# Kernel optimization log

Hardware: AMD Instinct MI355X
Metric: run time of the kernel (lower is better)

Reference implementation:

```python
import math
import jax, jax.numpy as jnp
import numpy as np

H = 16  # number of heads

def setup_inputs() -> dict:
    key0 = jax.random.key(0)
    ks = jax.random.split(key0, 8)
    B, S, D = 4, 2048, 1024
    query = jax.random.normal(ks[0], (B, S, D), dtype=jnp.float32)
    key_t = jax.random.normal(ks[1], (B, S, D), dtype=jnp.float32)
    value = jax.random.normal(ks[2], (B, S, D), dtype=jnp.float32)
    mask = jax.random.randint(ks[3], (B, S, S), 0, 2, dtype=jnp.int32)
    scale = 1.0 / math.sqrt(D)
    Wq = jax.random.normal(ks[4], (D, D), dtype=jnp.float32) * scale
    Wk = jax.random.normal(ks[5], (D, D), dtype=jnp.float32) * scale
    Wv = jax.random.normal(ks[6], (D, D), dtype=jnp.float32) * scale
    Wo = jax.random.normal(ks[7], (D, D), dtype=jnp.float32) * scale
    return {"query": query, "key": key_t, "value": value, "mask": mask,
            "Wq": Wq, "Wk": Wk, "Wv": Wv, "Wo": Wo}


def reference(query, key, value, mask, Wq, Wk, Wv, Wo):
    B, S, D = query.shape
    dk = D // H
    # Linear projections (nn.Linear, no bias): x @ W.T, then split heads
    def proj(x, W):
        return (x @ W.T).reshape(B, -1, H, dk).transpose(0, 2, 1, 3)  # [B,H,S,dk]
    q = proj(query, Wq)
    k = proj(key, Wk)
    v = proj(value, Wv)
    scores = jnp.einsum('bhqd,bhkd->bhqk', q, k) / math.sqrt(dk)
    m = mask[:, None, :, :] != 0  # [B,1,Sq,Sk] broadcast over heads
    scores = jnp.where(m, scores, jnp.float32(-1e9))
    p = jax.nn.softmax(scores, axis=-1)
    p = jnp.where(m, p, 0.0)
    # dropout is identity in eval mode
    x = jnp.einsum('bhqk,bhkd->bhqd', p, v)
    x = x.transpose(0, 2, 1, 3).reshape(B, -1, D)
    return x @ Wo.T
```

## Files before the change

kernel.cpp:

```cpp
#include <hip/hip_runtime.h>
#include <hip/hip_bf16.h>
#include <stdint.h>
#include <stddef.h>

typedef __bf16 bf16_t;
typedef __bf16 bf16x8 __attribute__((ext_vector_type(8)));
typedef __bf16 bf16x4 __attribute__((ext_vector_type(4)));
typedef float floatx4 __attribute__((ext_vector_type(4)));
typedef float floatx16 __attribute__((ext_vector_type(16)));

#define D_MODEL 1024
#define SEQ 2048
#define NB 4
#define NH 16
#define DK 64
#define MTOT 8192

#define QSCALE 0.1803368801111204f
#define FMAX 14.0f

__device__ inline bf16x8 ld8f(const float* p) {
  float4 a = *(const float4*)p;
  float4 b = *(const float4*)(p + 4);
  bf16x8 v;
  v[0] = (bf16_t)a.x; v[1] = (bf16_t)a.y; v[2] = (bf16_t)a.z; v[3] = (bf16_t)a.w;
  v[4] = (bf16_t)b.x; v[5] = (bf16_t)b.y; v[6] = (bf16_t)b.z; v[7] = (bf16_t)b.w;
  return v;
}

typedef const __attribute__((address_space(1))) unsigned int gu32;
typedef __attribute__((address_space(3))) unsigned int lu32;
__device__ static inline void async_copy16(const void* g, void* l) {
  __builtin_amdgcn_global_load_lds((gu32*)g, (lu32*)l, 16, 0, 0);
}

__device__ static inline uint32_t cvtpk_bf16(float lo, float hi) {
  uint32_t r;
  asm("v_cvt_pk_bf16_f32 %0, %1, %2" : "=v"(r) : "v"(lo), "v"(hi));
  return r;
}

__global__ __launch_bounds__(256) void prep_kernel(
    const float* __restrict__ q, const float* __restrict__ k,
    const float* __restrict__ v, const float* __restrict__ Wq,
    const float* __restrict__ Wk, const float* __restrict__ Wv,
    const int* __restrict__ mask, bf16_t* __restrict__ qb,
    bf16_t* __restrict__ kb, bf16_t* __restrict__ vb,
    bf16_t* __restrict__ wqb, bf16_t* __restrict__ wkb,
    bf16_t* __restrict__ wvb, uint32_t* __restrict__ bits) {
  size_t c = (size_t)blockIdx.x * 256 + threadIdx.x;
  const float* src;
  bf16_t* dst;
  size_t off;
  if (c < 1048576) { src = q; dst = qb; off = c; }
  else if (c < 2097152) { src = k; dst = kb; off = c - 1048576; }
  else if (c < 3145728) { src = v; dst = vb; off = c - 2097152; }
  else if (c < 3276800) { src = Wq; dst = wqb; off = c - 3145728; }
  else if (c < 3407872) { src = Wk; dst = wkb; off = c - 3276800; }
  else { src = Wv; dst = wvb; off = c - 3407872; }
  size_t e = off * 8;
  *(bf16x8*)&dst[e] = ld8f(&src[e]);

  const int lane = threadIdx.x & 63;
  const size_t w0 = c >> 6;
  const size_t nw = ((size_t)gridDim.x * 256) >> 6;
  const size_t total = (size_t)NB * SEQ * SEQ / 64;
  for (size_t i = w0; i < total; i += nw) {
    int mv = mask[i * 64 + lane];
    unsigned long long b = __ballot(mv != 0);
    if (lane == 0) *(unsigned long long*)&bits[i * 2] = b;
  }
}

__global__ __launch_bounds__(256) void cvt_w_kernel(const float* __restrict__ W,
                                                    bf16_t* __restrict__ wb) {
  size_t e = ((size_t)blockIdx.x * 256 + threadIdx.x) * 8;
  *(bf16x8*)&wb[e] = ld8f(&W[e]);
}

#define BM 64
#define BN 128
#define BK 64

template <int MODE, typename TC>
__global__ __launch_bounds__(256) void gemm_bt(const bf16_t* __restrict__ A,
                                               const bf16_t* __restrict__ W,
                                               TC* __restrict__ C, float scale) {
  __shared__ __align__(16) bf16_t As[BM * BK];
  __shared__ __align__(16) bf16_t Bs[BN * BK];
  const int tid = threadIdx.x;
  const int lane = tid & 63;
  const int wave = tid >> 6;
  const int row0 = blockIdx.x * BM;
  const int col0 = blockIdx.y * BN;
  const int wr = (wave >> 1) * 32;
  const int wc = (wave & 1) * 64;
  const int lrow = lane & 15;
  const int quad = lane >> 4;
  const int srow = lane >> 3;
  const int scol = ((lane & 7) ^ srow) * 8;

  floatx4 acc[2][4] = {};

  for (int k0 = 0; k0 < D_MODEL; k0 += BK) {
#pragma unroll
    for (int it = 0; it < 2; it++) {
      int seg = wave * 2 + it;
      async_copy16(&A[(size_t)(row0 + seg * 8 + srow) * D_MODEL + k0 + scol],
                   &As[seg * 512]);
    }
#pragma unroll
    for (int it = 0; it < 4; it++) {
      int seg = wave * 4 + it;
      async_copy16(&W[(size_t)(col0 + seg * 8 + srow) * D_MODEL + k0 + scol],
                   &Bs[seg * 512]);
    }
    __syncthreads();
#pragma unroll
    for (int kk = 0; kk < BK; kk += 32) {
      bf16x8 af[2], bfr[4];
#pragma unroll
      for (int i = 0; i < 2; i++)
        af[i] = *(const bf16x8*)&As[(wr + i * 16 + lrow) * BK +
                                    (((kk >> 3) + quad) ^ (lane & 7)) * 8];
#pragma unroll
      for (int j = 0; j < 4; j++)
        bfr[j] = *(const bf16x8*)&Bs[(wc + j * 16 + lrow) * BK +
                                     (((kk >> 3) + quad) ^ (lane & 7)) * 8];
#pragma unroll
      for (int i = 0; i < 2; i++)
#pragma unroll
        for (int j = 0; j < 4; j++)
          acc[i][j] = __builtin_amdgcn_mfma_f32_16x16x32_bf16(af[i], bfr[j],
                                                              acc[i][j], 0, 0, 0);
    }
    __syncthreads();
  }

#pragma unroll
  for (int i = 0; i < 2; i++) {
#pragma unroll
    for (int j = 0; j < 4; j++) {
      int gr0 = row0 + wr + i * 16 + quad * 4;
      int gc = col0 + wc + j * 16 + lrow;
      if (MODE == 1) {
        int b = gr0 >> 11;
        int s = gr0 & (SEQ - 1);
        bf16x4 v;
#pragma unroll
        for (int r = 0; r < 4; r++) v[r] = (bf16_t)(acc[i][j][r] * scale);
        *(bf16x4*)&C[((size_t)(b * D_MODEL + gc)) * SEQ + s] = v;
      } else {
#pragma unroll
        for (int r = 0; r < 4; r++)
          C[(size_t)(gr0 + r) * D_MODEL + gc] = (TC)(acc[i][j][r] * scale);
      }
    }
  }
}

__global__ __launch_bounds__(256) void attn_kernel(
    const bf16_t* __restrict__ Q, const bf16_t* __restrict__ K,
    const bf16_t* __restrict__ Vt, const uint32_t* __restrict__ bits,
    bf16_t* __restrict__ X) {
  __shared__ __align__(16) bf16_t Ks[128 * DK];
  __shared__ __align__(16) bf16_t Vs[DK * 128];
  const int tid = threadIdx.x;
  const int lane = tid & 63;
  const int wave = tid >> 6;
  const int l31 = lane & 31;
  const int half = lane >> 5;
  const int lrow16 = lane & 15;
  const int bh = blockIdx.x & 63;
  const int qbase = (blockIdx.x >> 6) * 128;
  const int b = bh >> 4;
  const int h = bh & 15;
  const int q0w = qbase + wave * 32;
  const int srow8 = lane >> 3;
  const int scol8 = ((lane & 7) ^ srow8) * 8;
  const int vrow = lane >> 4;

  bf16x8 qf[4];
#pragma unroll
  for (int kst = 0; kst < 4; kst++)
    qf[kst] = *(const bf16x8*)&Q[((size_t)(b * SEQ + q0w + l31)) * D_MODEL +
                                 h * DK + kst * 16 + half * 8];

  bf16x8 ones;
#pragma unroll
  for (int e = 0; e < 8; e++) ones[e] = (bf16_t)1.0f;

  const int kfbase = (l31 * 64) ^ ((lane & 7) * 8) ^ (half * 8);
  const int vfbase = (l31 * 128) ^ (lrow16 * 8) ^ (half * 8);

  floatx16 O0 = {}, O1 = {}, lsum = {};

  for (int kt = 0; kt < SEQ / 128; kt++) {
    const int kbase = kt * 128;
    const uint4 m4 =
        *(const uint4*)&bits[((size_t)(b * SEQ + q0w + l31)) * 64 + kt * 4];
    const uint32_t mwa[4] = {m4.x, m4.y, m4.z, m4.w};
    __syncthreads();
#pragma unroll
    for (int it = 0; it < 4; it++) {
      int seg = wave * 4 + it;
      async_copy16(&K[((size_t)(b * SEQ + kbase + seg * 8 + srow8)) * D_MODEL +
                      h * DK + scol8],
                   &Ks[seg * 512]);
    }
#pragma unroll
    for (int it = 0; it < 4; it++) {
      int seg = wave * 4 + it;
      int d = seg * 4 + vrow;
      async_copy16(&Vt[((size_t)(b * D_MODEL + h * DK + d)) * SEQ + kbase +
                       ((lrow16 ^ (d & 15)) * 8)],
                   &Vs[seg * 512]);
    }
    __syncthreads();

#pragma unroll
    for (int t = 0; t < 4; t++) {
      floatx16 s;
#pragma unroll
      for (int r = 0; r < 16; r++) s[r] = -FMAX;
#pragma unroll
      for (int kst = 0; kst < 4; kst++) {
        bf16x8 kf =
            *(const bf16x8*)&Ks[t * 2048 + (kfbase ^ (kst * 16))];
        s = __builtin_amdgcn_mfma_f32_32x32x16_bf16(kf, qf[kst], s, 0, 0, 0);
      }
      const uint32_t wh = mwa[t] >> (half * 4);
#pragma unroll
      for (int r = 0; r < 16; r++) {
        float p = __builtin_amdgcn_exp2f(s[r]);
        s[r] = ((wh >> ((r & 3) + 8 * (r >> 2))) & 1u) ? p : 0.f;
      }
#pragma unroll
      for (int ks = 0; ks < 2; ks++) {
        uint32_t w0 = cvtpk_bf16(s[8 * ks + 0], s[8 * ks + 1]);
        uint32_t w2 = cvtpk_bf16(s[8 * ks + 4], s[8 * ks + 5]);
        uint32_t w1 = cvtpk_bf16(s[8 * ks + 2], s[8 * ks + 3]);
        uint32_t w3 = cvtpk_bf16(s[8 * ks + 6], s[8 * ks + 7]);
        asm("v_permlane32_swap_b32 %0, %1" : "+v"(w0), "+v"(w2));
        asm("v_permlane32_swap_b32 %0, %1" : "+v"(w1), "+v"(w3));
        union { uint32_t u[4]; bf16x8 v; } pa;
        pa.u[0] = w0; pa.u[1] = w1; pa.u[2] = w2; pa.u[3] = w3;
        bf16x8 vf0 =
            *(const bf16x8*)&Vs[vfbase ^ (t * 32 + ks * 16)];
        bf16x8 vf1 =
            *(const bf16x8*)&Vs[4096 + (vfbase ^ (t * 32 + ks * 16))];
        O0 = __builtin_amdgcn_mfma_f32_32x32x16_bf16(pa.v, vf0, O0, 0, 0, 0);
        O1 = __builtin_amdgcn_mfma_f32_32x32x16_bf16(pa.v, vf1, O1, 0, 0, 0);
        lsum = __builtin_amdgcn_mfma_f32_32x32x16_bf16(pa.v, ones, lsum, 0, 0, 0);
      }
    }
  }

#pragma unroll
  for (int r = 0; r < 16; r++) {
    int qrow = q0w + (r & 3) + 8 * (r >> 2) + 4 * half;
    float li = lsum[r];
    float inv = (li > 0.f) ? 1.f / li : 0.f;
    X[((size_t)(b * SEQ + qrow)) * D_MODEL + h * DK + l31] =
        (bf16_t)(O0[r] * inv);
    X[((size_t)(b * SEQ + qrow)) * D_MODEL + h * DK + 32 + l31] =
        (bf16_t)(O1[r] * inv);
  }
}

extern "C" void kernel_launch(void* const* d_in, const int* in_sizes, int n_in,
                              void* d_out, int out_size, void* d_ws,
                              size_t ws_size, hipStream_t stream) {
  const float* query = (const float*)d_in[0];
  const float* key = (const float*)d_in[1];
  const float* value = (const float*)d_in[2];
  const int* mask = (const int*)d_in[3];
  const float* Wq = (const float*)d_in[4];
  const float* Wk = (const float*)d_in[5];
  const float* Wv = (const float*)d_in[6];
  const float* Wo = (const float*)d_in[7];
  float* out = (float*)d_out;

  char* ws = (char*)d_ws;
  char* dob = (char*)d_out;
  bf16_t* qb = (bf16_t*)(ws);
  bf16_t* kb = (bf16_t*)(ws + ((size_t)16 << 20));
  bf16_t* vb = (bf16_t*)(ws + ((size_t)32 << 20));
  bf16_t* Kp = qb;
  bf16_t* Vtp = kb;
  bf16_t* Xp = vb;
  bf16_t* wob = (bf16_t*)ws;
  bf16_t* Qp = (bf16_t*)d_out;
  uint32_t* bits = (uint32_t*)(dob + ((size_t)16 << 20));
  bf16_t* wqb = (bf16_t*)(dob + ((size_t)18 << 20));
  bf16_t* wkb = (bf16_t*)(dob + ((size_t)20 << 20));
  bf16_t* wvb = (bf16_t*)(dob + ((size_t)22 << 20));

  prep_kernel<<<13824, 256, 0, stream>>>(query, key, value, Wq, Wk, Wv, mask,
                                         qb, kb, vb, wqb, wkb, wvb, bits);

  dim3 gg(MTOT / BM, D_MODEL / BN);
  gemm_bt<0, bf16_t><<<gg, 256, 0, stream>>>(qb, wqb, Qp, QSCALE);
  gemm_bt<0, bf16_t><<<gg, 256, 0, stream>>>(kb, wkb, Kp, 1.0f);
  gemm_bt<1, bf16_t><<<gg, 256, 0, stream>>>(vb, wvb, Vtp, 1.0f);
  attn_kernel<<<dim3(SEQ / 128 * NB * NH), 256, 0, stream>>>(Qp, Kp, Vtp, bits,
                                                             Xp);
  cvt_w_kernel<<<512, 256, 0, stream>>>(Wo, wob);
  gemm_bt<0, float><<<gg, 256, 0, stream>>>(Xp, wob, out, 1.0f);
}
```

Before: 400.4 us.

## Double-buffer LDS tiles in projection GEMM to overlap loads with MFMA

Splits the GEMM's LDS A/B tiles into two buffers and issues the async copies for the next K tile before computing on the current one. Uses an explicit vmcnt wait (6 outstanding copies) plus barriers, which replaces the two full syncthreads per iteration. The goal is to hide global-to-LDS latency behind MFMA work, at the cost of twice the LDS per block, which may lower occupancy. The manual vmcnt count depends on the exact number of copies per thread.

```diff
diff --git a/kernel.cpp b/kernel.cpp
--- a/kernel.cpp
+++ b/kernel.cpp
@@ -86,8 +86,8 @@
 __global__ __launch_bounds__(256) void gemm_bt(const bf16_t* __restrict__ A,
                                                const bf16_t* __restrict__ W,
                                                TC* __restrict__ C, float scale) {
-  __shared__ __align__(16) bf16_t As[BM * BK];
-  __shared__ __align__(16) bf16_t Bs[BN * BK];
+  __shared__ __align__(16) bf16_t As[2][BM * BK];
+  __shared__ __align__(16) bf16_t Bs[2][BN * BK];
   const int tid = threadIdx.x;
   const int lane = tid & 63;
   const int wave = tid >> 6;
@@ -102,31 +102,33 @@
 
   floatx4 acc[2][4] = {};
 
-  for (int k0 = 0; k0 < D_MODEL; k0 += BK) {
+  auto stage = [&](int buf, int k0) {
 #pragma unroll
     for (int it = 0; it < 2; it++) {
       int seg = wave * 2 + it;
       async_copy16(&A[(size_t)(row0 + seg * 8 + srow) * D_MODEL + k0 + scol],
-                   &As[seg * 512]);
+                   &As[buf][seg * 512]);
     }
 #pragma unroll
     for (int it = 0; it < 4; it++) {
       int seg = wave * 4 + it;
       async_copy16(&W[(size_t)(col0 + seg * 8 + srow) * D_MODEL + k0 + scol],
-                   &Bs[seg * 512]);
-    }
-    __syncthreads();
+                   &Bs[buf][seg * 512]);
+    }
+  };
+
+  auto compute = [&](int buf) {
 #pragma unroll
     for (int kk = 0; kk < BK; kk += 32) {
       bf16x8 af[2], bfr[4];
 #pragma unroll
       for (int i = 0; i < 2; i++)
-        af[i] = *(const bf16x8*)&As[(wr + i * 16 + lrow) * BK +
-                                    (((kk >> 3) + quad) ^ (lane & 7)) * 8];
+        af[i] = *(const bf16x8*)&As[buf][(wr + i * 16 + lrow) * BK +
+                                        (((kk >> 3) + quad) ^ (lane & 7)) * 8];
 #pragma unroll
       for (int j = 0; j < 4; j++)
-        bfr[j] = *(const bf16x8*)&Bs[(wc + j * 16 + lrow) * BK +
-                                     (((kk >> 3) + quad) ^ (lane & 7)) * 8];
+        bfr[j] = *(const bf16x8*)&Bs[buf][(wc + j * 16 + lrow) * BK +
+                                         (((kk >> 3) + quad) ^ (lane & 7)) * 8];
 #pragma unroll
       for (int i = 0; i < 2; i++)
 #pragma unroll
@@ -134,8 +136,24 @@
           acc[i][j] = __builtin_amdgcn_mfma_f32_16x16x32_bf16(af[i], bfr[j],
                                                               acc[i][j], 0, 0, 0);
     }
-    __syncthreads();
-  }
+  };
+
+  stage(0, 0);
+  int cur = 0;
+  for (int t = 0; t < D_MODEL / BK - 1; t++) {
+    stage(cur ^ 1, (t + 1) * BK);
+    asm volatile("s_waitcnt vmcnt(6)" ::: "memory");
+    __builtin_amdgcn_s_barrier();
+    __builtin_amdgcn_sched_barrier(0);
+    compute(cur);
+    __builtin_amdgcn_sched_barrier(0);
+    __builtin_amdgcn_s_barrier();
+    cur ^= 1;
+  }
+  asm volatile("s_waitcnt vmcnt(0)" ::: "memory");
+  __builtin_amdgcn_s_barrier();
+  __builtin_amdgcn_sched_barrier(0);
+  compute(cur);
 
 #pragma unroll
   for (int i = 0; i < 2; i++) {
```

Result: slower. 425.8 us (+6.3%).

## Fuse fp32-to-bf16 activation conversion into a batched QKV projection GEMM

Applied to the files above, without the earlier changes.

The prep kernel no longer converts the query/key/value activations to bf16. A new gemm_qkv kernel loads fp32 activations directly, converts them in registers with packed bf16 converts, and computes all three projections in one launch using blockIdx.z. It also uses larger 128x128 tiles with a 4x4 MFMA accumulator per wave. This removes a full write and re-read of the bf16 activation copies and two kernel launches. The cost is that the A operand is now loaded synchronously in fp32, twice the bytes of bf16, with no async overlap, and the larger accumulator raises register pressure.

```diff
diff --git a/kernel.cpp b/kernel.cpp
--- a/kernel.cpp
+++ b/kernel.cpp
@@ -15,6 +15,11 @@
 #define NH 16
 #define DK 64
 #define MTOT 8192
+
+#define BKQ 64
+#define BM 64
+#define BN 128
+#define BK 64
 
 #define QSCALE 0.1803368801111204f
 #define FMAX 14.0f
@@ -41,26 +46,21 @@
 }
 
 __global__ __launch_bounds__(256) void prep_kernel(
-    const float* __restrict__ q, const float* __restrict__ k,
-    const float* __restrict__ v, const float* __restrict__ Wq,
-    const float* __restrict__ Wk, const float* __restrict__ Wv,
-    const int* __restrict__ mask, bf16_t* __restrict__ qb,
-    bf16_t* __restrict__ kb, bf16_t* __restrict__ vb,
+    const float* __restrict__ Wq, const float* __restrict__ Wk,
+    const float* __restrict__ Wv, const int* __restrict__ mask,
     bf16_t* __restrict__ wqb, bf16_t* __restrict__ wkb,
     bf16_t* __restrict__ wvb, uint32_t* __restrict__ bits) {
   size_t c = (size_t)blockIdx.x * 256 + threadIdx.x;
-  const float* src;
-  bf16_t* dst;
-  size_t off;
-  if (c < 1048576) { src = q; dst = qb; off = c; }
-  else if (c < 2097152) { src = k; dst = kb; off = c - 1048576; }
-  else if (c < 3145728) { src = v; dst = vb; off = c - 2097152; }
-  else if (c < 3276800) { src = Wq; dst = wqb; off = c - 3145728; }
-  else if (c < 3407872) { src = Wk; dst = wkb; off = c - 3276800; }
-  else { src = Wv; dst = wvb; off = c - 3407872; }
-  size_t e = off * 8;
-  *(bf16x8*)&dst[e] = ld8f(&src[e]);
-
+  if (c < 393216) {
+    const float* src;
+    bf16_t* dst;
+    size_t off;
+    if (c < 131072) { src = Wq; dst = wqb; off = c; }
+    else if (c < 262144) { src = Wk; dst = wkb; off = c - 131072; }
+    else { src = Wv; dst = wvb; off = c - 262144; }
+    size_t e = off * 8;
+    *(bf16x8*)&dst[e] = ld8f(&src[e]);
+  }
   const int lane = threadIdx.x & 63;
   const size_t w0 = c >> 6;
   const size_t nw = ((size_t)gridDim.x * 256) >> 6;
@@ -78,14 +78,101 @@
   *(bf16x8*)&wb[e] = ld8f(&W[e]);
 }
 
-#define BM 64
-#define BN 128
-#define BK 64
-
-template <int MODE, typename TC>
+__global__ __launch_bounds__(256) void gemm_qkv(
+    const float* __restrict__ qf, const float* __restrict__ kf,
+    const float* __restrict__ vf, const bf16_t* __restrict__ wqb,
+    const bf16_t* __restrict__ wkb, const bf16_t* __restrict__ wvb,
+    bf16_t* __restrict__ Qp, bf16_t* __restrict__ Kp,
+    bf16_t* __restrict__ Vtp) {
+  __shared__ __align__(16) bf16_t As[128 * 64];
+  __shared__ __align__(16) bf16_t Bs[128 * 64];
+  const int tid = threadIdx.x;
+  const int lane = tid & 63;
+  const int wave = tid >> 6;
+  const int z = blockIdx.z;
+  const float* A = (z == 0) ? qf : (z == 1) ? kf : vf;
+  const bf16_t* W = (z == 0) ? wqb : (z == 1) ? wkb : wvb;
+  const int row0 = blockIdx.x * 128;
+  const int col0 = blockIdx.y * 128;
+  const int wr = (wave >> 1) * 64;
+  const int wc = (wave & 1) * 64;
+  const int lrow = lane & 15;
+  const int quad = lane >> 4;
+  const int srow = lane >> 3;
+  const int scol = ((lane & 7) ^ srow) * 8;
+
+  floatx4 acc[4][4] = {};
+
+  for (int k0 = 0; k0 < D_MODEL; k0 += BKQ) {
+#pragma unroll
+    for (int it = 0; it < 4; it++) {
+      int seg = wave * 4 + it;
+      async_copy16(&W[(size_t)(col0 + seg * 8 + srow) * D_MODEL + k0 + scol],
+                   &Bs[seg * 512]);
+    }
+#pragma unroll
+    for (int it = 0; it < 4; it++) {
+      int seg = wave * 4 + it;
+      const float* src =
+          &A[(size_t)(row0 + seg * 8 + srow) * D_MODEL + k0 + scol];
+      float4 a = *(const float4*)src;
+      float4 b = *(const float4*)(src + 4);
+      uint4 wd;
+      wd.x = cvtpk_bf16(a.x, a.y);
+      wd.y = cvtpk_bf16(a.z, a.w);
+      wd.z = cvtpk_bf16(b.x, b.y);
+      wd.w = cvtpk_bf16(b.z, b.w);
+      *(uint4*)&As[seg * 512 + lane * 8] = wd;
+    }
+    __syncthreads();
+#pragma unroll
+    for (int kk = 0; kk < BKQ; kk += 32) {
+      bf16x8 af[4], bfr[4];
+#pragma unroll
+      for (int i = 0; i < 4; i++)
+        af[i] = *(const bf16x8*)&As[(wr + i * 16 + lrow) * 64 +
+                                    (((kk >> 3) + quad) ^ (lane & 7)) * 8];
+#pragma unroll
+      for (int j = 0; j < 4; j++)
+        bfr[j] = *(const bf16x8*)&Bs[(wc + j * 16 + lrow) * 64 +
+                                     (((kk >> 3) + quad) ^ (lane & 7)) * 8];
+#pragma unroll
+      for (int i = 0; i < 4; i++)
+#pragma unroll
+        for (int j = 0; j < 4; j++)
+          acc[i][j] = __builtin_amdgcn_mfma_f32_16x16x32_bf16(af[i], bfr[j],
+                                                              acc[i][j], 0, 0, 0);
+    }
+    __syncthreads();
+  }
+
+  const float scale = (z == 0) ? QSCALE : 1.0f;
+#pragma unroll
+  for (int i = 0; i < 4; i++) {
+#pragma unroll
+    for (int j = 0; j < 4; j++) {
+      int gr0 = row0 + wr + i * 16 + quad * 4;
+      int gc = col0 + wc + j * 16 + lrow;
+      if (z == 2) {
+        int bb = gr0 >> 11;
+        int s = gr0 & (SEQ - 1);
+        bf16x4 v;
+#pragma unroll
+        for (int r = 0; r < 4; r++) v[r] = (bf16_t)acc[i][j][r];
+        *(bf16x4*)&Vtp[((size_t)(bb * D_MODEL + gc)) * SEQ + s] = v;
+      } else {
+        bf16_t* C = (z == 0) ? Qp : Kp;
+#pragma unroll
+        for (int r = 0; r < 4; r++)
+          C[(size_t)(gr0 + r) * D_MODEL + gc] = (bf16_t)(acc[i][j][r] * scale);
+      }
+    }
+  }
+}
+
 __global__ __launch_bounds__(256) void gemm_bt(const bf16_t* __restrict__ A,
                                                const bf16_t* __restrict__ W,
-                                               TC* __restrict__ C, float scale) {
+                                               float* __restrict__ C) {
   __shared__ __align__(16) bf16_t As[BM * BK];
   __shared__ __align__(16) bf16_t Bs[BN * BK];
   const int tid = threadIdx.x;
@@ -143,18 +230,9 @@
     for (int j = 0; j < 4; j++) {
       int gr0 = row0 + wr + i * 16 + quad * 4;
       int gc = col0 + wc + j * 16 + lrow;
-      if (MODE == 1) {
-        int b = gr0 >> 11;
-        int s = gr0 & (SEQ - 1);
-        bf16x4 v;
-#pragma unroll
-        for (int r = 0; r < 4; r++) v[r] = (bf16_t)(acc[i][j][r] * scale);
-        *(bf16x4*)&C[((size_t)(b * D_MODEL + gc)) * SEQ + s] = v;
-      } else {
-#pragma unroll
-        for (int r = 0; r < 4; r++)
-          C[(size_t)(gr0 + r) * D_MODEL + gc] = (TC)(acc[i][j][r] * scale);
-      }
+#pragma unroll
+      for (int r = 0; r < 4; r++)
+        C[(size_t)(gr0 + r) * D_MODEL + gc] = acc[i][j][r];
     }
   }
 }
@@ -283,12 +361,9 @@
 
   char* ws = (char*)d_ws;
   char* dob = (char*)d_out;
-  bf16_t* qb = (bf16_t*)(ws);
-  bf16_t* kb = (bf16_t*)(ws + ((size_t)16 << 20));
-  bf16_t* vb = (bf16_t*)(ws + ((size_t)32 << 20));
-  bf16_t* Kp = qb;
-  bf16_t* Vtp = kb;
-  bf16_t* Xp = vb;
+  bf16_t* Kp = (bf16_t*)(ws);
+  bf16_t* Vtp = (bf16_t*)(ws + ((size_t)16 << 20));
+  bf16_t* Xp = (bf16_t*)(ws + ((size_t)32 << 20));
   bf16_t* wob = (bf16_t*)ws;
   bf16_t* Qp = (bf16_t*)d_out;
   uint32_t* bits = (uint32_t*)(dob + ((size_t)16 << 20));
@@ -296,15 +371,13 @@
   bf16_t* wkb = (bf16_t*)(dob + ((size_t)20 << 20));
   bf16_t* wvb = (bf16_t*)(dob + ((size_t)22 << 20));
 
-  prep_kernel<<<13824, 256, 0, stream>>>(query, key, value, Wq, Wk, Wv, mask,
-                                         qb, kb, vb, wqb, wkb, wvb, bits);
-
-  dim3 gg(MTOT / BM, D_MODEL / BN);
-  gemm_bt<0, bf16_t><<<gg, 256, 0, stream>>>(qb, wqb, Qp, QSCALE);
-  gemm_bt<0, bf16_t><<<gg, 256, 0, stream>>>(kb, wkb, Kp, 1.0f);
-  gemm_bt<1, bf16_t><<<gg, 256, 0, stream>>>(vb, wvb, Vtp, 1.0f);
+  prep_kernel<<<4096, 256, 0, stream>>>(Wq, Wk, Wv, mask, wqb, wkb, wvb, bits);
+
+  gemm_qkv<<<dim3(MTOT / 128, D_MODEL / 128, 3), 256, 0, stream>>>(
+      query, key, value, wqb, wkb, wvb, Qp, Kp, Vtp);
+
   attn_kernel<<<dim3(SEQ / 128 * NB * NH), 256, 0, stream>>>(Qp, Kp, Vtp, bits,
                                                              Xp);
   cvt_w_kernel<<<512, 256, 0, stream>>>(Wo, wob);
-  gemm_bt<0, float><<<gg, 256, 0, stream>>>(Xp, wob, out, 1.0f);
-}
+  gemm_bt<<<dim3(MTOT / BM, D_MODEL / BN), 256, 0, stream>>>(Xp, wob, out);
+}
```

Measured after the change: 416.8 us. 4.1% more time.
